# Kernel tuning notes

Measured on AMD Instinct MI355X. Metric: run time of the kernel, lower is better.

## Reference

```python
import jax, jax.numpy as jnp
import numpy as np

S, B, D, H = 2048, 8, 512, 8
HD = D // H

def setup_inputs() -> dict:
    key = jax.random.key(0)
    ks = jax.random.split(key, 5)
    return {
        "src": jax.random.normal(ks[0], (S, B, D), dtype=jnp.float32),
        "in_proj_w": jax.random.normal(ks[1], (3 * D, D), dtype=jnp.float32) * (D ** -0.5),
        "in_proj_b": jax.random.normal(ks[2], (3 * D,), dtype=jnp.float32) * 0.02,
        "out_w": jax.random.normal(ks[3], (D, D), dtype=jnp.float32) * (D ** -0.5),
        "out_b": jax.random.normal(ks[4], (D,), dtype=jnp.float32) * 0.02,
    }

def reference(src, in_proj_w, in_proj_b, out_w, out_b):
    s, b, d = src.shape
    h, hd = H, HD
    # packed qkv projection: [S,B,3D]
    qkv = src @ in_proj_w.T + in_proj_b
    q, k, v = jnp.split(qkv, 3, axis=-1)
    # [S,B,H,hd]
    q = q.reshape(s, b, h, hd) * (hd ** -0.5)
    k = k.reshape(s, b, h, hd)
    v = v.reshape(s, b, h, hd)
    # scores [B,H,S,S]
    scores = jnp.einsum("sbhd,tbhd->bhst", q, k)
    attn = jax.nn.softmax(scores, axis=-1)
    # context [S,B,D]
    ctx = jnp.einsum("bhst,tbhd->sbhd", attn, v).reshape(s, b, d)
    out = ctx @ out_w.T + out_b
    # torch averages attention weights over heads when need_weights=True
    attn_weights = attn.mean(axis=1)  # [B,S,S]
    return out, attn_weights
```

## Files before the change

### kernel.cpp

```cpp
#include <hip/hip_runtime.h>
#include <hip/hip_bf16.h>

#define S_LEN 2048
#define BATCH 8
#define DMODEL 512
#define NHEAD 8
#define HDIM 64

#define QSCALE 0.18033688011112042f

typedef unsigned short u16;
typedef __bf16 bf16_t;
typedef bf16_t bf16x8 __attribute__((ext_vector_type(8)));
typedef float f32x4 __attribute__((ext_vector_type(4)));
typedef float f32x16 __attribute__((ext_vector_type(16)));
typedef u16 u16x8 __attribute__((ext_vector_type(8)));
typedef u16 u16x4 __attribute__((ext_vector_type(4)));
typedef unsigned u32x4 __attribute__((ext_vector_type(4)));

__device__ __forceinline__ u16 f2bf(float f) {
    unsigned u = __float_as_uint(f);
    u = (u + 0x7fffu + ((u >> 16) & 1u)) >> 16;
    return (u16)u;
}

__device__ __forceinline__ bf16x8 ld_frag(const u16* p) {
    u16x8 v = *(const u16x8*)p;
    return __builtin_bit_cast(bf16x8, v);
}

#define MFMA16(a, b, c) __builtin_amdgcn_mfma_f32_16x16x32_bf16((a), (b), (c), 0, 0, 0)
#define MFMA32(a, b, c) __builtin_amdgcn_mfma_f32_32x32x16_bf16((a), (b), (c), 0, 0, 0)
#define EXP2F(x) __builtin_amdgcn_exp2f(x)

__device__ __forceinline__ unsigned cvtpk(float lo, float hi) {
    unsigned r;
    asm("v_cvt_pk_bf16_f32 %0, %1, %2" : "=v"(r) : "v"(lo), "v"(hi));
    return r;
}
__device__ __forceinline__ void swap32(unsigned& a, unsigned& b) {
    asm("v_permlane32_swap_b32 %0, %1" : "+v"(a), "+v"(b));
}

__global__ __launch_bounds__(256) void cast_weights(const float* __restrict__ wq,
                                                    const float* __restrict__ wo,
                                                    u16* __restrict__ dst) {
    int i = (blockIdx.x * 256 + threadIdx.x) * 4;
    float4 v;
    if (i < 786432) v = *(const float4*)(wq + i);
    else            v = *(const float4*)(wo + (i - 786432));
    u16x4 o = {f2bf(v.x), f2bf(v.y), f2bf(v.z), f2bf(v.w)};
    *(u16x4*)(dst + i) = o;
}

__global__ __launch_bounds__(256) void qkv_gemm(const float* __restrict__ src,
                                                const u16* __restrict__ Wq,
                                                const float* __restrict__ bias,
                                                u16* __restrict__ Qs,
                                                u16* __restrict__ Ks,
                                                u16* __restrict__ Vs) {
    __shared__ u16 Al[128][40];
    __shared__ u16 Bl[128][40];
    const int tid = threadIdx.x;
    const int lane = tid & 63, wid = tid >> 6;
    const int m0 = blockIdx.y * 128, n0 = blockIdx.x * 128;
    const int lr = lane & 15, lkg = lane >> 4, lk = lkg * 8;
    const int wr = (wid >> 1) * 64, wc = (wid & 1) * 64;
    const int ar = tid >> 1, ac = (tid & 1) * 16;

    f32x4 acc[4][4];
#pragma unroll
    for (int i = 0; i < 4; i++)
#pragma unroll
        for (int n = 0; n < 4; n++) acc[i][n] = (f32x4){0.f, 0.f, 0.f, 0.f};

    for (int k0 = 0; k0 < DMODEL; k0 += 32) {
        __syncthreads();
        {
            const float* sp = src + (size_t)(m0 + ar) * DMODEL + k0 + ac;
            float4 v0 = *(const float4*)(sp + 0);
            float4 v1 = *(const float4*)(sp + 4);
            float4 v2 = *(const float4*)(sp + 8);
            float4 v3 = *(const float4*)(sp + 12);
            u16x8 p0 = {f2bf(v0.x), f2bf(v0.y), f2bf(v0.z), f2bf(v0.w),
                        f2bf(v1.x), f2bf(v1.y), f2bf(v1.z), f2bf(v1.w)};
            u16x8 p1 = {f2bf(v2.x), f2bf(v2.y), f2bf(v2.z), f2bf(v2.w),
                        f2bf(v3.x), f2bf(v3.y), f2bf(v3.z), f2bf(v3.w)};
            *(u16x8*)&Al[ar][ac] = p0;
            *(u16x8*)&Al[ar][ac + 8] = p1;
            const u16* wp = Wq + (size_t)(n0 + ar) * DMODEL + k0 + ac;
            *(u16x8*)&Bl[ar][ac] = *(const u16x8*)wp;
            *(u16x8*)&Bl[ar][ac + 8] = *(const u16x8*)(wp + 8);
        }
        __syncthreads();
        bf16x8 af[4], bfr[4];
#pragma unroll
        for (int i = 0; i < 4; i++) af[i] = ld_frag(&Al[wr + i * 16 + lr][lk]);
#pragma unroll
        for (int n = 0; n < 4; n++) bfr[n] = ld_frag(&Bl[wc + n * 16 + lr][lk]);
#pragma unroll
        for (int i = 0; i < 4; i++)
#pragma unroll
            for (int n = 0; n < 4; n++) acc[i][n] = MFMA16(af[i], bfr[n], acc[i][n]);
    }

    float bv[4];
#pragma unroll
    for (int n = 0; n < 4; n++) bv[n] = bias[n0 + wc + n * 16 + lr];
#pragma unroll
    for (int i = 0; i < 4; i++) {
#pragma unroll
        for (int n = 0; n < 4; n++) {
            int ncol = n0 + wc + n * 16 + lr;
            int sect = ncol >> 9, idx = ncol & 511;
            int h = idx >> 6, d = idx & 63;
#pragma unroll
            for (int j = 0; j < 4; j++) {
                int m = m0 + wr + i * 16 + lkg * 4 + j;
                int srow = m >> 3, bidx = m & 7;
                float val = acc[i][n][j] + bv[n];
                size_t o = (((size_t)(bidx * NHEAD + h) * S_LEN) + srow) * HDIM + d;
                if (sect == 0)      Qs[o] = f2bf(val * QSCALE);
                else if (sect == 1) Ks[o] = f2bf(val);
                else                Vs[o] = f2bf(val);
            }
        }
    }
}

__global__ __launch_bounds__(256) void transpose_v(const u16* __restrict__ Vs,
                                                   u16* __restrict__ Vt) {
    __shared__ u16 tile[64][70];
    int bh = blockIdx.y, t0 = blockIdx.x * 64;
    int tid = threadIdx.x;
    int r = tid >> 2, c = (tid & 3) * 16;
    const u16* vp = Vs + ((size_t)bh * S_LEN + t0 + r) * HDIM + c;
    u16x8 x0 = *(const u16x8*)vp;
    u16x8 x1 = *(const u16x8*)(vp + 8);
#pragma unroll
    for (int i = 0; i < 8; i++) tile[r][c + i] = x0[i];
#pragma unroll
    for (int i = 0; i < 8; i++) tile[r][c + 8 + i] = x1[i];
    __syncthreads();
    int d0 = tid >> 2, tt = (tid & 3) * 16;
    u16x8 y0, y1;
#pragma unroll
    for (int i = 0; i < 8; i++) y0[i] = tile[tt + i][d0];
#pragma unroll
    for (int i = 0; i < 8; i++) y1[i] = tile[tt + 8 + i][d0];
    u16* op = Vt + ((size_t)bh * HDIM + d0) * S_LEN + t0 + tt;
    *(u16x8*)op = y0;
    *(u16x8*)(op + 8) = y1;
}

__global__ __launch_bounds__(256) void ctx_kernel(const u16* __restrict__ Qs,
                                                  const u16* __restrict__ Ks,
                                                  const u16* __restrict__ Vt,
                                                  float* __restrict__ Lr,
                                                  u16* __restrict__ Ctx) {
    __shared__ char lds[32768];
    __shared__ float cjl[4][32];
    const int tid = threadIdx.x, lane = tid & 63, wid = tid >> 6;
    const int l31 = lane & 31, hi = lane >> 5;
    const int bh = blockIdx.y, b = bh >> 3, h = bh & 7;
    const int q0w = blockIdx.x * 128 + wid * 32;
    const u16* Qb = Qs + (size_t)bh * S_LEN * HDIM;
    const u16* Kb = Ks + (size_t)bh * S_LEN * HDIM;
    const u16* Vb = Vt + (size_t)bh * HDIM * S_LEN;

    bf16x8 qf[4];
#pragma unroll
    for (int kc = 0; kc < 4; kc++)
        qf[kc] = ld_frag(Qb + (size_t)(q0w + l31) * HDIM + kc * 16 + hi * 8);

    const int o0 = tid * 32;
    const int srow = o0 >> 7, scol = o0 & 127;
    const int p0 = srow * 128 + (scol ^ ((srow & 7) << 4));
    const int p1 = srow * 128 + ((scol + 16) ^ ((srow & 7) << 4));
    const char* Ksrc = (const char*)Kb + (size_t)srow * 128 + scol;
    const char* Vsrc = (const char*)(Vb + (size_t)srow * S_LEN) + scol;

    u16x8 sreg0, sreg1, sreg2, sreg3;
    sreg0 = *(const u16x8*)(Ksrc);
    sreg1 = *(const u16x8*)(Ksrc + 16);
    sreg2 = *(const u16x8*)(Vsrc);
    sreg3 = *(const u16x8*)(Vsrc + 16);
    *(u16x8*)(lds + p0) = sreg0;
    *(u16x8*)(lds + p1) = sreg1;
    *(u16x8*)(lds + 8192 + p0) = sreg2;
    *(u16x8*)(lds + 8192 + p1) = sreg3;
    __syncthreads();

    f32x16 cacc0, cacc1;
#pragma unroll
    for (int r = 0; r < 16; r++) { cacc0[r] = 0.f; cacc1[r] = 0.f; }
    float lsum = 0.f;
    int buf = 0;

    for (int it = 0; it < 32; ++it) {
        if (it < 31) {
            const char* kn = Ksrc + (size_t)(it + 1) * 8192;
            const char* vn = Vsrc + (size_t)(it + 1) * 128;
            sreg0 = *(const u16x8*)(kn);
            sreg1 = *(const u16x8*)(kn + 16);
            sreg2 = *(const u16x8*)(vn);
            sreg3 = *(const u16x8*)(vn + 16);
        }
        const char* Kl = lds + buf * 16384;
        const char* Vl = Kl + 8192;

        f32x16 st0, st1;
#pragma unroll
        for (int r = 0; r < 16; r++) { st0[r] = 0.f; st1[r] = 0.f; }
        __builtin_amdgcn_s_setprio(1);
#pragma unroll
        for (int kc = 0; kc < 4; kc++) {
            int row0 = l31, row1 = 32 + l31;
            int c = kc * 32 + hi * 16;
            bf16x8 a0 = *(const bf16x8*)(Kl + row0 * 128 + (c ^ ((row0 & 7) << 4)));
            bf16x8 a1 = *(const bf16x8*)(Kl + row1 * 128 + (c ^ ((row1 & 7) << 4)));
            st0 = MFMA32(a0, qf[kc], st0);
            st1 = MFMA32(a1, qf[kc], st1);
        }
        __builtin_amdgcn_s_setprio(0);

#pragma unroll
        for (int r = 0; r < 16; r++) {
            float e0 = EXP2F(st0[r]);
            float e1 = EXP2F(st1[r]);
            lsum += e0 + e1;
            st0[r] = e0;
            st1[r] = e1;
        }

        bf16x8 pa[4];
#pragma unroll
        for (int half = 0; half < 2; half++) {
            int h8 = half * 8;
            unsigned a0 = cvtpk(st0[h8 + 0], st0[h8 + 1]);
            unsigned b0 = cvtpk(st0[h8 + 4], st0[h8 + 5]);
            swap32(a0, b0);
            unsigned a1 = cvtpk(st0[h8 + 2], st0[h8 + 3]);
            unsigned b1 = cvtpk(st0[h8 + 6], st0[h8 + 7]);
            swap32(a1, b1);
            u32x4 w = {a0, a1, b0, b1};
            pa[half] = __builtin_bit_cast(bf16x8, w);
        }
#pragma unroll
        for (int half = 0; half < 2; half++) {
            int h8 = half * 8;
            unsigned a0 = cvtpk(st1[h8 + 0], st1[h8 + 1]);
            unsigned b0 = cvtpk(st1[h8 + 4], st1[h8 + 5]);
            swap32(a0, b0);
            unsigned a1 = cvtpk(st1[h8 + 2], st1[h8 + 3]);
            unsigned b1 = cvtpk(st1[h8 + 6], st1[h8 + 7]);
            swap32(a1, b1);
            u32x4 w = {a0, a1, b0, b1};
            pa[2 + half] = __builtin_bit_cast(bf16x8, w);
        }

        __builtin_amdgcn_s_setprio(1);
#pragma unroll
        for (int ks = 0; ks < 4; ks++) {
            int c = ks * 32 + hi * 16;
            int row0 = l31, row1 = 32 + l31;
            bf16x8 v0 = *(const bf16x8*)(Vl + row0 * 128 + (c ^ ((row0 & 7) << 4)));
            bf16x8 v1 = *(const bf16x8*)(Vl + row1 * 128 + (c ^ ((row1 & 7) << 4)));
            cacc0 = MFMA32(pa[ks], v0, cacc0);
            cacc1 = MFMA32(pa[ks], v1, cacc1);
        }
        __builtin_amdgcn_s_setprio(0);

        if (it < 31) {
            char* d = lds + (buf ^ 1) * 16384;
            *(u16x8*)(d + p0) = sreg0;
            *(u16x8*)(d + p1) = sreg1;
            *(u16x8*)(d + 8192 + p0) = sreg2;
            *(u16x8*)(d + 8192 + p1) = sreg3;
        }
        __syncthreads();
        buf ^= 1;
    }

    float tot = lsum + __shfl_xor(lsum, 32);
    float cj = 1.0f / tot;
    if (hi == 0) {
        Lr[(size_t)bh * S_LEN + q0w + l31] = cj;
        cjl[wid][l31] = cj;
    }
    float cjr[16];
#pragma unroll
    for (int r = 0; r < 16; r++)
        cjr[r] = cjl[wid][(r & 3) + 8 * (r >> 2) + 4 * hi];

#pragma unroll
    for (int r = 0; r < 16; r++) {
        int q = q0w + (r & 3) + 8 * (r >> 2) + 4 * hi;
        size_t base = ((size_t)q * BATCH + b) * DMODEL + h * 64;
        Ctx[base + l31] = f2bf(cacc0[r] * cjr[r]);
        Ctx[base + 32 + l31] = f2bf(cacc1[r] * cjr[r]);
    }
}

__global__ __launch_bounds__(256) void mean_kernel(const u16* __restrict__ Qs,
                                                   const u16* __restrict__ Ks,
                                                   const float* __restrict__ Lr,
                                                   float* __restrict__ attnw) {
    __shared__ u16 Kl[64][72];
    int b = blockIdx.y;
    int r0 = (blockIdx.x & 31) * 64, t0 = (blockIdx.x >> 5) * 64;
    int tid = threadIdx.x, lane = tid & 63, wid = tid >> 6;
    int lr = lane & 15, lkg = lane >> 4, lk = lkg * 8;
    int kr = tid >> 2, kc = (tid & 3) * 16;

    float cjh[8][4];
#pragma unroll
    for (int h = 0; h < 8; h++)
#pragma unroll
        for (int j = 0; j < 4; j++)
            cjh[h][j] = 0.125f *
                Lr[(size_t)(b * 8 + h) * S_LEN + r0 + wid * 16 + lkg * 4 + j];

    f32x4 macc[4];
#pragma unroll
    for (int n = 0; n < 4; n++) macc[n] = (f32x4){0.f, 0.f, 0.f, 0.f};

#pragma unroll
    for (int h = 0; h < 8; h++) {
        int bh = b * 8 + h;
        const u16* Qb = Qs + (size_t)bh * S_LEN * HDIM;
        const u16* Kb = Ks + (size_t)bh * S_LEN * HDIM;
        __syncthreads();
        {
            const u16* kp = Kb + (size_t)(t0 + kr) * HDIM + kc;
            *(u16x8*)&Kl[kr][kc] = *(const u16x8*)kp;
            *(u16x8*)&Kl[kr][kc + 8] = *(const u16x8*)(kp + 8);
        }
        __syncthreads();
        bf16x8 a0 = ld_frag(Qb + (size_t)(r0 + wid * 16 + lr) * HDIM + lk);
        bf16x8 a1 = ld_frag(Qb + (size_t)(r0 + wid * 16 + lr) * HDIM + 32 + lk);
        f32x4 sc[4];
#pragma unroll
        for (int n = 0; n < 4; n++) sc[n] = (f32x4){0.f, 0.f, 0.f, 0.f};
#pragma unroll
        for (int n = 0; n < 4; n++) {
            bf16x8 b0 = ld_frag(&Kl[n * 16 + lr][lk]);
            bf16x8 b1 = ld_frag(&Kl[n * 16 + lr][32 + lk]);
            sc[n] = MFMA16(a0, b0, sc[n]);
            sc[n] = MFMA16(a1, b1, sc[n]);
        }
#pragma unroll
        for (int n = 0; n < 4; n++)
#pragma unroll
            for (int j = 0; j < 4; j++)
                macc[n][j] += EXP2F(sc[n][j]) * cjh[h][j];
    }

#pragma unroll
    for (int n = 0; n < 4; n++)
#pragma unroll
        for (int j = 0; j < 4; j++) {
            int row = r0 + wid * 16 + lkg * 4 + j;
            attnw[((size_t)b * S_LEN + row) * S_LEN + t0 + n * 16 + lr] = macc[n][j];
        }
}

__global__ __launch_bounds__(256) void out_gemm(const u16* __restrict__ Ctx,
                                                const u16* __restrict__ Wo,
                                                const float* __restrict__ obias,
                                                float* __restrict__ out) {
    __shared__ u16 Al[128][40];
    __shared__ u16 Bl[128][40];
    const int tid = threadIdx.x;
    const int lane = tid & 63, wid = tid >> 6;
    const int m0 = blockIdx.y * 128, n0 = blockIdx.x * 128;
    const int lr = lane & 15, lkg = lane >> 4, lk = lkg * 8;
    const int wr = (wid >> 1) * 64, wc = (wid & 1) * 64;
    const int ar = tid >> 1, ac = (tid & 1) * 16;

    f32x4 acc[4][4];
#pragma unroll
    for (int i = 0; i < 4; i++)
#pragma unroll
        for (int n = 0; n < 4; n++) acc[i][n] = (f32x4){0.f, 0.f, 0.f, 0.f};

    for (int k0 = 0; k0 < DMODEL; k0 += 32) {
        __syncthreads();
        {
            const u16* apz = Ctx + (size_t)(m0 + ar) * DMODEL + k0 + ac;
            *(u16x8*)&Al[ar][ac] = *(const u16x8*)apz;
            *(u16x8*)&Al[ar][ac + 8] = *(const u16x8*)(apz + 8);
            const u16* wp = Wo + (size_t)(n0 + ar) * DMODEL + k0 + ac;
            *(u16x8*)&Bl[ar][ac] = *(const u16x8*)wp;
            *(u16x8*)&Bl[ar][ac + 8] = *(const u16x8*)(wp + 8);
        }
        __syncthreads();
        bf16x8 af[4], bfr[4];
#pragma unroll
        for (int i = 0; i < 4; i++) af[i] = ld_frag(&Al[wr + i * 16 + lr][lk]);
#pragma unroll
        for (int n = 0; n < 4; n++) bfr[n] = ld_frag(&Bl[wc + n * 16 + lr][lk]);
#pragma unroll
        for (int i = 0; i < 4; i++)
#pragma unroll
            for (int n = 0; n < 4; n++) acc[i][n] = MFMA16(af[i], bfr[n], acc[i][n]);
    }

    float bv[4];
#pragma unroll
    for (int n = 0; n < 4; n++) bv[n] = obias[n0 + wc + n * 16 + lr];
#pragma unroll
    for (int i = 0; i < 4; i++)
#pragma unroll
        for (int n = 0; n < 4; n++) {
            int ncol = n0 + wc + n * 16 + lr;
#pragma unroll
            for (int j = 0; j < 4; j++) {
                int m = m0 + wr + i * 16 + lkg * 4 + j;
                out[(size_t)m * DMODEL + ncol] = acc[i][n][j] + bv[n];
            }
        }
}

extern "C" void kernel_launch(void* const* d_in, const int* in_sizes, int n_in,
                              void* d_out, int out_size, void* d_ws, size_t ws_size,
                              hipStream_t stream) {
    const float* src   = (const float*)d_in[0];
    const float* w_in  = (const float*)d_in[1];
    const float* b_in  = (const float*)d_in[2];
    const float* w_out = (const float*)d_in[3];
    const float* b_out = (const float*)d_in[4];
    float* out = (float*)d_out;
    float* attnw = out + (size_t)S_LEN * BATCH * DMODEL;

    float* Lr = (float*)d_ws;
    u16* Wqb = (u16*)(Lr + 131072);
    u16* Wob = Wqb + 786432;
    u16* Qs  = Wob + 262144;
    u16* Ks  = Qs + 8388608;
    u16* Vs  = Ks + 8388608;
    u16* Vt  = Vs + 8388608;
    u16* Ctx = Vt + 8388608;

    cast_weights<<<dim3(1024), dim3(256), 0, stream>>>(w_in, w_out, Wqb);
    qkv_gemm<<<dim3(12, 128), dim3(256), 0, stream>>>(src, Wqb, b_in, Qs, Ks, Vs);
    transpose_v<<<dim3(32, 64), dim3(256), 0, stream>>>(Vs, Vt);
    ctx_kernel<<<dim3(16, 64), dim3(256), 0, stream>>>(Qs, Ks, Vt, Lr, Ctx);
    mean_kernel<<<dim3(1024, 8), dim3(256), 0, stream>>>(Qs, Ks, Lr, attnw);
    out_gemm<<<dim3(4, 128), dim3(256), 0, stream>>>(Ctx, Wob, b_out, out);
}
```

Baseline: 457.8 us.

## Enlarge mean_kernel tile to 128 query rows and batch K loads per four heads

The head-averaged attention-weight kernel now covers 128 query rows per block instead of 64, so each wave handles two 16-row groups that reuse the same K fragments held in registers. K tiles for four heads are staged into a 32KB XOR-swizzled shared-memory buffer at once, which cuts the barriers from two per head to about two per four heads and avoids LDS bank conflicts. The per-head 1/L scaling is now loaded as vectors inside the loop rather than precomputed for all heads. The intent is to halve redundant K global loads and reduce synchronization. The cost is higher register and LDS use, which may lower occupancy, and half as many blocks are launched.

```diff
diff --git a/kernel.cpp b/kernel.cpp
--- a/kernel.cpp
+++ b/kernel.cpp
@@ -306,63 +306,101 @@
                                                    const u16* __restrict__ Ks,
                                                    const float* __restrict__ Lr,
                                                    float* __restrict__ attnw) {
-    __shared__ u16 Kl[64][72];
-    int b = blockIdx.y;
-    int r0 = (blockIdx.x & 31) * 64, t0 = (blockIdx.x >> 5) * 64;
-    int tid = threadIdx.x, lane = tid & 63, wid = tid >> 6;
-    int lr = lane & 15, lkg = lane >> 4, lk = lkg * 8;
-    int kr = tid >> 2, kc = (tid & 3) * 16;
-
-    float cjh[8][4];
-#pragma unroll
-    for (int h = 0; h < 8; h++)
-#pragma unroll
-        for (int j = 0; j < 4; j++)
-            cjh[h][j] = 0.125f *
-                Lr[(size_t)(b * 8 + h) * S_LEN + r0 + wid * 16 + lkg * 4 + j];
-
-    f32x4 macc[4];
-#pragma unroll
-    for (int n = 0; n < 4; n++) macc[n] = (f32x4){0.f, 0.f, 0.f, 0.f};
-
-#pragma unroll
-    for (int h = 0; h < 8; h++) {
-        int bh = b * 8 + h;
-        const u16* Qb = Qs + (size_t)bh * S_LEN * HDIM;
-        const u16* Kb = Ks + (size_t)bh * S_LEN * HDIM;
-        __syncthreads();
-        {
-            const u16* kp = Kb + (size_t)(t0 + kr) * HDIM + kc;
-            *(u16x8*)&Kl[kr][kc] = *(const u16x8*)kp;
-            *(u16x8*)&Kl[kr][kc + 8] = *(const u16x8*)(kp + 8);
-        }
-        __syncthreads();
-        bf16x8 a0 = ld_frag(Qb + (size_t)(r0 + wid * 16 + lr) * HDIM + lk);
-        bf16x8 a1 = ld_frag(Qb + (size_t)(r0 + wid * 16 + lr) * HDIM + 32 + lk);
-        f32x4 sc[4];
-#pragma unroll
-        for (int n = 0; n < 4; n++) sc[n] = (f32x4){0.f, 0.f, 0.f, 0.f};
-#pragma unroll
-        for (int n = 0; n < 4; n++) {
-            bf16x8 b0 = ld_frag(&Kl[n * 16 + lr][lk]);
-            bf16x8 b1 = ld_frag(&Kl[n * 16 + lr][32 + lk]);
-            sc[n] = MFMA16(a0, b0, sc[n]);
-            sc[n] = MFMA16(a1, b1, sc[n]);
-        }
+    __shared__ char lds[32768];
+    const int b = blockIdx.y;
+    const int r0 = (blockIdx.x & 15) * 128, t0 = (blockIdx.x >> 4) * 64;
+    const int tid = threadIdx.x, lane = tid & 63, wid = tid >> 6;
+    const int lr = lane & 15, lkg = lane >> 4;
+    const int swz = (lr & 7) << 4;
+    const int qrow0 = r0 + wid * 32;
+
+    const int o0 = tid * 32;
+    const int srow = o0 >> 7, scol = o0 & 127;
+    const int d0 = srow * 128 + (scol ^ ((srow & 7) << 4));
+    const int d1 = srow * 128 + ((scol + 16) ^ ((srow & 7) << 4));
+
+    f32x4 macc[2][4];
+#pragma unroll
+    for (int g = 0; g < 2; g++)
+#pragma unroll
+        for (int n = 0; n < 4; n++) macc[g][n] = (f32x4){0.f, 0.f, 0.f, 0.f};
+
+    for (int rd = 0; rd < 2; ++rd) {
+        if (rd) __syncthreads();
+#pragma unroll
+        for (int h = 0; h < 4; ++h) {
+            const char* kp = (const char*)(Ks +
+                (size_t)((b * NHEAD + rd * 4 + h) * S_LEN + t0) * HDIM) + o0;
+            u16x8 c0 = *(const u16x8*)kp;
+            u16x8 c1 = *(const u16x8*)(kp + 16);
+            char* dst = lds + h * 8192;
+            *(u16x8*)(dst + d0) = c0;
+            *(u16x8*)(dst + d1) = c1;
+        }
+        __syncthreads();
+#pragma unroll
+        for (int h = 0; h < 4; ++h) {
+            const int bh = b * NHEAD + rd * 4 + h;
+            const u16* Qb = Qs + (size_t)bh * S_LEN * HDIM;
+            const char* Kl = lds + h * 8192;
+
+            bf16x8 bb0[4], bb1[4];
+#pragma unroll
+            for (int n = 0; n < 4; n++) {
+                int row = n * 16 + lr;
+                bb0[n] = *(const bf16x8*)(Kl + row * 128 + ((lkg * 16) ^ swz));
+                bb1[n] = *(const bf16x8*)(Kl + row * 128 + ((64 + lkg * 16) ^ swz));
+            }
+            f32x4 cj0 = 0.125f * *(const f32x4*)(Lr + (size_t)bh * S_LEN + qrow0 + lkg * 4);
+            f32x4 cj1 = 0.125f * *(const f32x4*)(Lr + (size_t)bh * S_LEN + qrow0 + 16 + lkg * 4);
+
+            {
+                bf16x8 a0 = ld_frag(Qb + (size_t)(qrow0 + lr) * HDIM + lkg * 8);
+                bf16x8 a1 = ld_frag(Qb + (size_t)(qrow0 + lr) * HDIM + 32 + lkg * 8);
+                f32x4 sc[4];
+#pragma unroll
+                for (int n = 0; n < 4; n++) sc[n] = (f32x4){0.f, 0.f, 0.f, 0.f};
+#pragma unroll
+                for (int n = 0; n < 4; n++) {
+                    sc[n] = MFMA16(a0, bb0[n], sc[n]);
+                    sc[n] = MFMA16(a1, bb1[n], sc[n]);
+                }
+#pragma unroll
+                for (int n = 0; n < 4; n++)
+#pragma unroll
+                    for (int j = 0; j < 4; j++)
+                        macc[0][n][j] += EXP2F(sc[n][j]) * cj0[j];
+            }
+            {
+                bf16x8 a0 = ld_frag(Qb + (size_t)(qrow0 + 16 + lr) * HDIM + lkg * 8);
+                bf16x8 a1 = ld_frag(Qb + (size_t)(qrow0 + 16 + lr) * HDIM + 32 + lkg * 8);
+                f32x4 sc[4];
+#pragma unroll
+                for (int n = 0; n < 4; n++) sc[n] = (f32x4){0.f, 0.f, 0.f, 0.f};
+#pragma unroll
+                for (int n = 0; n < 4; n++) {
+                    sc[n] = MFMA16(a0, bb0[n], sc[n]);
+                    sc[n] = MFMA16(a1, bb1[n], sc[n]);
+                }
+#pragma unroll
+                for (int n = 0; n < 4; n++)
+#pragma unroll
+                    for (int j = 0; j < 4; j++)
+                        macc[1][n][j] += EXP2F(sc[n][j]) * cj1[j];
+            }
+        }
+    }
+
+#pragma unroll
+    for (int g = 0; g < 2; g++)
 #pragma unroll
         for (int n = 0; n < 4; n++)
 #pragma unroll
-            for (int j = 0; j < 4; j++)
-                macc[n][j] += EXP2F(sc[n][j]) * cjh[h][j];
-    }
-
-#pragma unroll
-    for (int n = 0; n < 4; n++)
-#pragma unroll
-        for (int j = 0; j < 4; j++) {
-            int row = r0 + wid * 16 + lkg * 4 + j;
-            attnw[((size_t)b * S_LEN + row) * S_LEN + t0 + n * 16 + lr] = macc[n][j];
-        }
+            for (int j = 0; j < 4; j++) {
+                int row = qrow0 + g * 16 + lkg * 4 + j;
+                attnw[((size_t)b * S_LEN + row) * S_LEN + t0 + n * 16 + lr] =
+                    macc[g][n][j];
+            }
 }
 
 __global__ __launch_bounds__(256) void out_gemm(const u16* __restrict__ Ctx,
@@ -446,6 +484,6 @@
     qkv_gemm<<<dim3(12, 128), dim3(256), 0, stream>>>(src, Wqb, b_in, Qs, Ks, Vs);
     transpose_v<<<dim3(32, 64), dim3(256), 0, stream>>>(Vs, Vt);
     ctx_kernel<<<dim3(16, 64), dim3(256), 0, stream>>>(Qs, Ks, Vt, Lr, Ctx);
-    mean_kernel<<<dim3(1024, 8), dim3(256), 0, stream>>>(Qs, Ks, Lr, attnw);
+    mean_kernel<<<dim3(512, 8), dim3(256), 0, stream>>>(Qs, Ks, Lr, attnw);
     out_gemm<<<dim3(4, 128), dim3(256), 0, stream>>>(Ctx, Wob, b_out, out);
 }
```

Result: no change. 461.4 us (+0.8%).
